# Kernel tuning notes

Hardware: AMD Instinct MI355X
Metric: run time of the kernel (lower is better)

Reference implementation:

```python
import jax, jax.numpy as jnp
import numpy as np

# Reconstructed from DAT's DAttentionBaseline with the wrapper's config:
# q_size=(14,14), n_heads=12, n_head_channels=64, n_groups=8, stride=1,
# offset_range_factor=1.0, use_pe=False (so log_cpb/rpe unused), no_off=False,
# ksize=3, dropout=0 (eval). Followed by the wrapper's Linear out-projection.

H = W = 14
G = 8          # n_groups
NH = 12        # n_heads
OFF_RANGE_FACTOR = 1.0


def grid_sample_bilinear(img, grid):
    # img: [B, C, H, W]; grid: [B, Hg, Wg, 2] in (x, y) order, [-1, 1],
    # align_corners=True, padding_mode='zeros' (torch defaults used by DAT).
    B, C, Hi, Wi = img.shape
    gx = (grid[..., 0] + 1.0) * 0.5 * (Wi - 1)
    gy = (grid[..., 1] + 1.0) * 0.5 * (Hi - 1)
    x0 = jnp.floor(gx)
    y0 = jnp.floor(gy)
    x1 = x0 + 1.0
    y1 = y0 + 1.0
    wx1 = gx - x0
    wx0 = 1.0 - wx1
    wy1 = gy - y0
    wy0 = 1.0 - wy1
    flat = img.reshape(B, C, Hi * Wi)

    def tap(xi, yi, wgt):
        valid = (xi >= 0) & (xi <= Wi - 1) & (yi >= 0) & (yi <= Hi - 1)
        xi_c = jnp.clip(xi, 0, Wi - 1).astype(jnp.int32)
        yi_c = jnp.clip(yi, 0, Hi - 1).astype(jnp.int32)
        idx = (yi_c * Wi + xi_c).reshape(B, 1, -1)
        vals = jnp.take_along_axis(flat, idx, axis=2)  # [B, C, Hg*Wg]
        w = (wgt * valid.astype(img.dtype)).reshape(B, 1, -1)
        return vals * w

    out = (tap(x0, y0, wx0 * wy0) + tap(x1, y0, wx1 * wy0)
           + tap(x0, y1, wx0 * wy1) + tap(x1, y1, wx1 * wy1))
    return out  # [B, C, Hg*Wg]


def setup_inputs() -> dict:
    key = jax.random.key(0)
    ks = jax.random.split(key, 16)
    B, N, C = 128, 196, 768
    Cg = C // G  # 96
    s = 0.02
    return {
        "hidden_states": jax.random.normal(ks[0], (B, N, C), jnp.float32),
        "Wq": jax.random.normal(ks[1], (C, C), jnp.float32) * s,
        "bq": jnp.zeros((C,), jnp.float32),
        "off_dw_w": jax.random.normal(ks[2], (Cg, 1, 3, 3), jnp.float32) * s,
        "off_dw_b": jnp.zeros((Cg,), jnp.float32),
        "ln_w": jnp.ones((Cg,), jnp.float32),
        "ln_b": jnp.zeros((Cg,), jnp.float32),
        "off_pw_w": jax.random.normal(ks[3], (2, Cg), jnp.float32) * s,
        "Wk": jax.random.normal(ks[4], (C, C), jnp.float32) * s,
        "bk": jnp.zeros((C,), jnp.float32),
        "Wv": jax.random.normal(ks[5], (C, C), jnp.float32) * s,
        "bv": jnp.zeros((C,), jnp.float32),
        "Wproj": jax.random.normal(ks[6], (C, C), jnp.float32) * s,
        "bproj": jnp.zeros((C,), jnp.float32),
        "Wout": jax.random.normal(ks[7], (C, C), jnp.float32) * s,
        "bout": jnp.zeros((C,), jnp.float32),
    }


def reference(hidden_states, Wq, bq, off_dw_w, off_dw_b, ln_w, ln_b, off_pw_w,
              Wk, bk, Wv, bv, Wproj, bproj, Wout, bout):
    B, N, C = hidden_states.shape
    Cg = C // G
    nh, dh = NH, C // NH
    scale = dh ** -0.5
    dt = hidden_states.dtype

    x_im = hidden_states.reshape(B, H, W, C).transpose(0, 3, 1, 2)  # [B,C,H,W]

    # proj_q: 1x1 conv
    q_im = jnp.einsum('bchw,oc->bohw', x_im, Wq) + bq[None, :, None, None]
    q_off = q_im.reshape(B * G, Cg, H, W)

    # offset net: depthwise 3x3 conv -> LayerNorm(channels) -> GELU -> 1x1 (no bias)
    t = jax.lax.conv_general_dilated(
        q_off, off_dw_w, (1, 1), [(1, 1), (1, 1)],
        dimension_numbers=('NCHW', 'OIHW', 'NCHW'), feature_group_count=Cg)
    t = t + off_dw_b[None, :, None, None]
    mu = t.mean(axis=1, keepdims=True)
    var = ((t - mu) ** 2).mean(axis=1, keepdims=True)
    t = (t - mu) * jax.lax.rsqrt(var + 1e-5)
    t = t * ln_w[None, :, None, None] + ln_b[None, :, None, None]
    t = jax.nn.gelu(t, approximate=False)
    off = jnp.einsum('bchw,oc->bohw', t, off_pw_w)  # [B*G, 2(y,x), H, W]

    off_range = jnp.array([1.0 / (H - 1), 1.0 / (W - 1)], dt).reshape(1, 2, 1, 1)
    off = jnp.tanh(off) * off_range * OFF_RANGE_FACTOR
    off = off.transpose(0, 2, 3, 1)  # [B*G, H, W, 2] (y, x)

    ry = ((jnp.arange(H, dtype=dt) + 0.5) / H) * 2.0 - 1.0
    rx = ((jnp.arange(W, dtype=dt) + 0.5) / W) * 2.0 - 1.0
    ref = jnp.stack(jnp.meshgrid(ry, rx, indexing='ij'), axis=-1)  # [H,W,2]
    pos = off + ref[None]          # (y, x)
    grid = pos[..., ::-1]          # (x, y) for grid_sample

    x_g = x_im.reshape(B * G, Cg, H, W)
    n_sample = H * W
    x_s = grid_sample_bilinear(x_g, grid).reshape(B, C, n_sample)

    k = jnp.einsum('bcn,oc->bon', x_s, Wk) + bk[None, :, None]
    v = jnp.einsum('bcn,oc->bon', x_s, Wv) + bv[None, :, None]

    qh = q_im.reshape(B, nh, dh, N)
    kh = k.reshape(B, nh, dh, n_sample)
    vh = v.reshape(B, nh, dh, n_sample)

    attn = jax.nn.softmax(jnp.einsum('bhcm,bhcn->bhmn', qh, kh) * scale, axis=-1)
    out = jnp.einsum('bhmn,bhcn->bhcm', attn, vh).reshape(B, C, N)

    y = jnp.einsum('bcn,oc->bon', out, Wproj) + bproj[None, :, None]
    y = y.transpose(0, 2, 1)               # [B, N, C]
    y = y @ Wout.T + bout                  # wrapper's Linear out-projection
    return y, attn
```

## Files before the change

kernel.cpp:

```cpp
#include <hip/hip_runtime.h>
#include <math.h>

#define Bsz 128
#define Hh 14
#define Ww 14
#define Nn 196
#define Cc 768
#define Gg 8
#define CgC 96
#define NHh 12
#define Dh 64
#define ROWS (Bsz*Nn)

typedef _Float16 half8 __attribute__((ext_vector_type(8)));
typedef _Float16 half4 __attribute__((ext_vector_type(4)));
typedef float f32x4 __attribute__((ext_vector_type(4)));

__global__ __launch_bounds__(256) void cvt_w5(
    const float* __restrict__ w0, const float* __restrict__ w1,
    const float* __restrict__ w2, const float* __restrict__ w3,
    const float* __restrict__ w4, _Float16* __restrict__ dst)
{
  const int i = blockIdx.x * 256 + threadIdx.x;
  const int per = Cc * Cc / 8;
  if (i >= 5 * per) return;
  const int m = i / per, r = i - m * per;
  const float* s = (m == 0) ? w0 : (m == 1) ? w1 : (m == 2) ? w2 : (m == 3) ? w3 : w4;
  float4 a = *(const float4*)(s + (size_t)r * 8);
  float4 b = *(const float4*)(s + (size_t)r * 8 + 4);
  half8 h;
  h[0]=(_Float16)a.x; h[1]=(_Float16)a.y; h[2]=(_Float16)a.z; h[3]=(_Float16)a.w;
  h[4]=(_Float16)b.x; h[5]=(_Float16)b.y; h[6]=(_Float16)b.z; h[7]=(_Float16)b.w;
  *(half8*)(dst + (size_t)m * Cc * Cc + (size_t)r * 8) = h;
}

__global__ __launch_bounds__(256) void fuse_bias(
    const float* __restrict__ Wo, const float* __restrict__ bp,
    const float* __restrict__ bo, float* __restrict__ bf)
{
  __shared__ float red[256];
  const int o2 = blockIdx.x;
  const int tid = threadIdx.x;
  const float* wrow = Wo + (size_t)o2 * Cc;
  float s = 0.f;
  for (int o = tid; o < Cc; o += 256) s = fmaf(wrow[o], bp[o], s);
  red[tid] = s;
  __syncthreads();
  for (int st = 128; st > 0; st >>= 1) { if (tid < st) red[tid] += red[tid + st]; __syncthreads(); }
  if (tid == 0) bf[o2] = red[0] + bo[o2];
}

__global__ __launch_bounds__(256) void gemm_ww(
    const _Float16* __restrict__ Wo16, const _Float16* __restrict__ Wp16,
    _Float16* __restrict__ Wf)
{
  __shared__ __align__(16) _Float16 As[128 * 64];
  __shared__ __align__(16) _Float16 Bs[128 * 72];
  const int t = threadIdx.x;
  const int bid = blockIdx.x;
  const int colb = bid % 6, rowb = bid / 6;
  const int row0 = rowb * 128, col0 = colb * 128;
  const int lane = t & 63, w = t >> 6;
  const int wr = w >> 1, wc = w & 1;
  const int l15 = lane & 15, l4 = lane >> 4;
  const int srow = t >> 3;
  const int sg   = t & 7;

  f32x4 acc[4][4];
#pragma unroll
  for (int i = 0; i < 4; ++i)
#pragma unroll
    for (int j = 0; j < 4; ++j) acc[i][j] = (f32x4){0.f, 0.f, 0.f, 0.f};

  for (int kt = 0; kt < 12; ++kt) {
    const int k0 = kt * 64;
#pragma unroll
    for (int it = 0; it < 4; ++it) {
      const int r = it * 32 + srow;
      half8 ha = *(const half8*)(Wo16 + (size_t)(row0 + r) * Cc + k0 + sg * 8);
      *(half8*)&As[r * 64 + ((sg ^ (r & 7)) * 8)] = ha;
    }
    {
      const int og = t >> 4;
      const int cg = t & 15;
#pragma unroll
      for (int it = 0; it < 4; ++it) {
        const int o = it * 16 + og;
        half8 hv = *(const half8*)(Wp16 + (size_t)(k0 + o) * Cc + col0 + cg * 8);
#pragma unroll
        for (int e = 0; e < 8; ++e)
          Bs[(cg * 8 + e) * 72 + o] = hv[e];
      }
    }
    __syncthreads();
#pragma unroll
    for (int ks = 0; ks < 2; ++ks) {
      half8 af[4], bf[4];
#pragma unroll
      for (int mi = 0; mi < 4; ++mi) {
        const int r = wr * 64 + mi * 16 + l15;
        const int g = ks * 4 + l4;
        af[mi] = *(const half8*)&As[r * 64 + ((g ^ (r & 7)) * 8)];
      }
#pragma unroll
      for (int ni = 0; ni < 4; ++ni) {
        const int c = wc * 64 + ni * 16 + l15;
        bf[ni] = *(const half8*)&Bs[c * 72 + ks * 32 + l4 * 8];
      }
#pragma unroll
      for (int mi = 0; mi < 4; ++mi)
#pragma unroll
        for (int ni = 0; ni < 4; ++ni)
          acc[mi][ni] = __builtin_amdgcn_mfma_f32_16x16x32_f16(af[mi], bf[ni], acc[mi][ni], 0, 0, 0);
    }
    __syncthreads();
  }

#pragma unroll
  for (int ni = 0; ni < 4; ++ni) {
    const int col = col0 + wc * 64 + ni * 16 + l15;
#pragma unroll
    for (int mi = 0; mi < 4; ++mi) {
      f32x4 v = acc[mi][ni];
      const int rbase = row0 + wr * 64 + mi * 16 + l4 * 4;
#pragma unroll
      for (int r = 0; r < 4; ++r)
        Wf[(size_t)(rbase + r) * Cc + col] = (_Float16)v[r];
    }
  }
}

__global__ __launch_bounds__(256) void gemm_f32a(
    const float* __restrict__ A, const _Float16* __restrict__ W,
    const float* __restrict__ bias, _Float16* __restrict__ Cout)
{
  __shared__ __align__(16) _Float16 As[128 * 64];
  __shared__ __align__(16) _Float16 Bs[128 * 64];
  const int t = threadIdx.x;
  const int nwg = gridDim.x;
  int bid = blockIdx.x;
  bid = (bid & 7) * (nwg >> 3) + (bid >> 3);
  const int colb = bid % 6, rowb = bid / 6;
  const int row0 = rowb * 128, col0 = colb * 128;
  const int lane = t & 63, w = t >> 6;
  const int wr = w >> 1, wc = w & 1;
  const int l15 = lane & 15, l4 = lane >> 4;
  const int srow = t >> 3;
  const int sg   = t & 7;

  f32x4 acc[4][4];
#pragma unroll
  for (int i = 0; i < 4; ++i)
#pragma unroll
    for (int j = 0; j < 4; ++j) acc[i][j] = (f32x4){0.f, 0.f, 0.f, 0.f};

  for (int kt = 0; kt < 12; ++kt) {
    const int k0 = kt * 64;
#pragma unroll
    for (int it = 0; it < 4; ++it) {
      const int r = it * 32 + srow;
      const float* ap = A + (size_t)(row0 + r) * Cc + k0 + sg * 8;
      float4 a0 = *(const float4*)ap;
      float4 a1 = *(const float4*)(ap + 4);
      half8 ha;
      ha[0]=(_Float16)a0.x; ha[1]=(_Float16)a0.y; ha[2]=(_Float16)a0.z; ha[3]=(_Float16)a0.w;
      ha[4]=(_Float16)a1.x; ha[5]=(_Float16)a1.y; ha[6]=(_Float16)a1.z; ha[7]=(_Float16)a1.w;
      half8 hw = *(const half8*)(W + (size_t)(col0 + r) * Cc + k0 + sg * 8);
      const int dst = r * 64 + ((sg ^ (r & 7)) * 8);
      *(half8*)&As[dst] = ha;
      *(half8*)&Bs[dst] = hw;
    }
    __syncthreads();
#pragma unroll
    for (int ks = 0; ks < 2; ++ks) {
      half8 af[4], bf[4];
#pragma unroll
      for (int mi = 0; mi < 4; ++mi) {
        const int r = wr * 64 + mi * 16 + l15;
        const int g = ks * 4 + l4;
        af[mi] = *(const half8*)&As[r * 64 + ((g ^ (r & 7)) * 8)];
      }
#pragma unroll
      for (int ni = 0; ni < 4; ++ni) {
        const int r = wc * 64 + ni * 16 + l15;
        const int g = ks * 4 + l4;
        bf[ni] = *(const half8*)&Bs[r * 64 + ((g ^ (r & 7)) * 8)];
      }
#pragma unroll
      for (int mi = 0; mi < 4; ++mi)
#pragma unroll
        for (int ni = 0; ni < 4; ++ni)
          acc[mi][ni] = __builtin_amdgcn_mfma_f32_16x16x32_f16(af[mi], bf[ni], acc[mi][ni], 0, 0, 0);
    }
    __syncthreads();
  }

#pragma unroll
  for (int ni = 0; ni < 4; ++ni) {
    const int col = col0 + wc * 64 + ni * 16 + l15;
    const float bcol = bias[col];
#pragma unroll
    for (int mi = 0; mi < 4; ++mi) {
      f32x4 v = acc[mi][ni];
      const int rbase = row0 + wr * 64 + mi * 16 + l4 * 4;
#pragma unroll
      for (int r = 0; r < 4; ++r)
        Cout[(size_t)(rbase + r) * Cc + col] = (_Float16)(v[r] + bcol);
    }
  }
}

template<int F16OUT>
__global__ __launch_bounds__(256) void gemm_h16(
    const _Float16* __restrict__ A, const _Float16* __restrict__ W,
    const float* __restrict__ bias, void* __restrict__ Cout)
{
  __shared__ __align__(16) _Float16 As[128 * 64];
  __shared__ __align__(16) _Float16 Bs[128 * 64];
  const int t = threadIdx.x;
  const int nwg = gridDim.x;
  int bid = blockIdx.x;
  bid = (bid & 7) * (nwg >> 3) + (bid >> 3);
  const int colb = bid % 6, rowb = bid / 6;
  const int row0 = rowb * 128, col0 = colb * 128;
  const int lane = t & 63, w = t >> 6;
  const int wr = w >> 1, wc = w & 1;
  const int l15 = lane & 15, l4 = lane >> 4;
  const int srow = t >> 3;
  const int sg   = t & 7;

  f32x4 acc[4][4];
#pragma unroll
  for (int i = 0; i < 4; ++i)
#pragma unroll
    for (int j = 0; j < 4; ++j) acc[i][j] = (f32x4){0.f, 0.f, 0.f, 0.f};

  for (int kt = 0; kt < 12; ++kt) {
    const int k0 = kt * 64;
#pragma unroll
    for (int it = 0; it < 4; ++it) {
      const int r = it * 32 + srow;
      half8 ha = *(const half8*)(A + (size_t)(row0 + r) * Cc + k0 + sg * 8);
      half8 hw = *(const half8*)(W + (size_t)(col0 + r) * Cc + k0 + sg * 8);
      const int dst = r * 64 + ((sg ^ (r & 7)) * 8);
      *(half8*)&As[dst] = ha;
      *(half8*)&Bs[dst] = hw;
    }
    __syncthreads();
#pragma unroll
    for (int ks = 0; ks < 2; ++ks) {
      half8 af[4], bf[4];
#pragma unroll
      for (int mi = 0; mi < 4; ++mi) {
        const int r = wr * 64 + mi * 16 + l15;
        const int g = ks * 4 + l4;
        af[mi] = *(const half8*)&As[r * 64 + ((g ^ (r & 7)) * 8)];
      }
#pragma unroll
      for (int ni = 0; ni < 4; ++ni) {
        const int r = wc * 64 + ni * 16 + l15;
        const int g = ks * 4 + l4;
        bf[ni] = *(const half8*)&Bs[r * 64 + ((g ^ (r & 7)) * 8)];
      }
#pragma unroll
      for (int mi = 0; mi < 4; ++mi)
#pragma unroll
        for (int ni = 0; ni < 4; ++ni)
          acc[mi][ni] = __builtin_amdgcn_mfma_f32_16x16x32_f16(af[mi], bf[ni], acc[mi][ni], 0, 0, 0);
    }
    __syncthreads();
  }

#pragma unroll
  for (int ni = 0; ni < 4; ++ni) {
    const int col = col0 + wc * 64 + ni * 16 + l15;
    const float bcol = bias[col];
#pragma unroll
    for (int mi = 0; mi < 4; ++mi) {
      f32x4 v = acc[mi][ni];
      const int rbase = row0 + wr * 64 + mi * 16 + l4 * 4;
#pragma unroll
      for (int r = 0; r < 4; ++r) {
        if (F16OUT) {
          ((_Float16*)Cout)[(size_t)(rbase + r) * Cc + col] = (_Float16)(v[r] + bcol);
        } else {
          ((float*)Cout)[(size_t)(rbase + r) * Cc + col] = v[r] + bcol;
        }
      }
    }
  }
}

__global__ __launch_bounds__(256) void gemm_h16_kv(
    const _Float16* __restrict__ A, const _Float16* __restrict__ Wkv,
    const float* __restrict__ bk, const float* __restrict__ bv,
    _Float16* __restrict__ K16, _Float16* __restrict__ V16)
{
  __shared__ __align__(16) _Float16 As[128 * 64];
  __shared__ __align__(16) _Float16 Bs[128 * 64];
  const int t = threadIdx.x;
  const int nwg = gridDim.x;
  int bid = blockIdx.x;
  bid = (bid & 7) * (nwg >> 3) + (bid >> 3);
  const int colb = bid % 12, rowb = bid / 12;
  const int row0 = rowb * 128, col0 = colb * 128;
  const int lane = t & 63, w = t >> 6;
  const int wr = w >> 1, wc = w & 1;
  const int l15 = lane & 15, l4 = lane >> 4;
  const int srow = t >> 3;
  const int sg   = t & 7;

  _Float16* Cout = (colb < 6) ? K16 : V16;
  const float* bias = (colb < 6) ? bk : bv;
  const int cadj = (colb < 6) ? 0 : Cc;

  f32x4 acc[4][4];
#pragma unroll
  for (int i = 0; i < 4; ++i)
#pragma unroll
    for (int j = 0; j < 4; ++j) acc[i][j] = (f32x4){0.f, 0.f, 0.f, 0.f};

  for (int kt = 0; kt < 12; ++kt) {
    const int k0 = kt * 64;
#pragma unroll
    for (int it = 0; it < 4; ++it) {
      const int r = it * 32 + srow;
      half8 ha = *(const half8*)(A + (size_t)(row0 + r) * Cc + k0 + sg * 8);
      half8 hw = *(const half8*)(Wkv + (size_t)(col0 + r) * Cc + k0 + sg * 8);
      const int dst = r * 64 + ((sg ^ (r & 7)) * 8);
      *(half8*)&As[dst] = ha;
      *(half8*)&Bs[dst] = hw;
    }
    __syncthreads();
#pragma unroll
    for (int ks = 0; ks < 2; ++ks) {
      half8 af[4], bf[4];
#pragma unroll
      for (int mi = 0; mi < 4; ++mi) {
        const int r = wr * 64 + mi * 16 + l15;
        const int g = ks * 4 + l4;
        af[mi] = *(const half8*)&As[r * 64 + ((g ^ (r & 7)) * 8)];
      }
#pragma unroll
      for (int ni = 0; ni < 4; ++ni) {
        const int r = wc * 64 + ni * 16 + l15;
        const int g = ks * 4 + l4;
        bf[ni] = *(const half8*)&Bs[r * 64 + ((g ^ (r & 7)) * 8)];
      }
#pragma unroll
      for (int mi = 0; mi < 4; ++mi)
#pragma unroll
        for (int ni = 0; ni < 4; ++ni)
          acc[mi][ni] = __builtin_amdgcn_mfma_f32_16x16x32_f16(af[mi], bf[ni], acc[mi][ni], 0, 0, 0);
    }
    __syncthreads();
  }

#pragma unroll
  for (int ni = 0; ni < 4; ++ni) {
    const int col = col0 + wc * 64 + ni * 16 + l15;
    const float bcol = bias[col - cadj];
#pragma unroll
    for (int mi = 0; mi < 4; ++mi) {
      f32x4 v = acc[mi][ni];
      const int rbase = row0 + wr * 64 + mi * 16 + l4 * 4;
#pragma unroll
      for (int r = 0; r < 4; ++r)
        Cout[(size_t)(rbase + r) * Cc + (col - cadj)] = (_Float16)(v[r] + bcol);
    }
  }
}

__global__ __launch_bounds__(512, 4) void offset_sample(
    const _Float16* __restrict__ Q16, const float* __restrict__ hidden,
    const float* __restrict__ dw_w, const float* __restrict__ dw_b,
    const float* __restrict__ ln_w, const float* __restrict__ ln_b,
    const float* __restrict__ pw_w, _Float16* __restrict__ XS)
{
  __shared__ float Qs[Nn * CgC];
  const int tid = threadIdx.x;
  const int g = blockIdx.x;
  const int b = blockIdx.y;
  const int cl = tid & 31;
  const int grp = tid >> 5;

  const size_t base = (size_t)b * Nn * Cc + g * CgC;
  for (int i = tid; i < Nn * 12; i += 512) {
    const int n = i / 12, j = i - n * 12;
    half8 hv = *(const half8*)(Q16 + base + (size_t)n * Cc + j * 8);
#pragma unroll
    for (int e = 0; e < 8; ++e) Qs[n * CgC + j * 8 + e] = (float)hv[e];
  }

  float wdw[3][9], bdw[3], wln[3], bln[3], wp0[3], wp1[3];
#pragma unroll
  for (int k = 0; k < 3; ++k) {
    const int c = cl + k * 32;
#pragma unroll
    for (int t9 = 0; t9 < 9; ++t9) wdw[k][t9] = dw_w[c * 9 + t9];
    bdw[k] = dw_b[c];
    wln[k] = ln_w[c];
    bln[k] = ln_b[c];
    wp0[k] = pw_w[c];
    wp1[k] = pw_w[CgC + c];
  }
  __syncthreads();

  const float* hb0 = hidden + base;

  for (int s0 = 0; s0 < Nn; s0 += 16) {
    const int site = s0 + grp;
    if (site >= Nn) break;
    const int h = site / Ww, w = site % Ww;

    float t[3];
#pragma unroll
    for (int k = 0; k < 3; ++k) t[k] = bdw[k];
#pragma unroll
    for (int ky = 0; ky < 3; ++ky) {
      const int hp = h + ky - 1;
      if (hp < 0 || hp > Hh - 1) continue;
#pragma unroll
      for (int kx = 0; kx < 3; ++kx) {
        const int wp = w + kx - 1;
        if (wp < 0 || wp > Ww - 1) continue;
        const float* row = &Qs[(hp * Ww + wp) * CgC + cl];
#pragma unroll
        for (int k = 0; k < 3; ++k)
          t[k] = fmaf(row[k * 32], wdw[k][ky * 3 + kx], t[k]);
      }
    }

    float s = t[0] + t[1] + t[2];
#pragma unroll
    for (int off = 1; off <= 16; off <<= 1) s += __shfl_xor(s, off, 32);
    const float mu = s * (1.f / 96.f);
    float d2 = 0.f;
#pragma unroll
    for (int k = 0; k < 3; ++k) { const float d = t[k] - mu; d2 = fmaf(d, d, d2); }
#pragma unroll
    for (int off = 1; off <= 16; off <<= 1) d2 += __shfl_xor(d2, off, 32);
    const float rstd = rsqrtf(d2 * (1.f / 96.f) + 1e-5f);

    float p0 = 0.f, p1 = 0.f;
#pragma unroll
    for (int k = 0; k < 3; ++k) {
      const float tn = (t[k] - mu) * rstd * wln[k] + bln[k];
      const float a = 0.5f * tn * (1.f + erff(tn * 0.70710678118654752f));
      p0 = fmaf(a, wp0[k], p0);
      p1 = fmaf(a, wp1[k], p1);
    }
#pragma unroll
    for (int off = 1; off <= 16; off <<= 1) {
      p0 += __shfl_xor(p0, off, 32);
      p1 += __shfl_xor(p1, off, 32);
    }

    const float offy = tanhf(p0) * (1.f / 13.f);
    const float offx = tanhf(p1) * (1.f / 13.f);
    const float refy = (h + 0.5f) / 14.f * 2.f - 1.f;
    const float refx = (w + 0.5f) / 14.f * 2.f - 1.f;
    const float gx = ((offx + refx) + 1.f) * 0.5f * 13.f;
    const float gy = ((offy + refy) + 1.f) * 0.5f * 13.f;

    const float x0f = floorf(gx), y0f = floorf(gy);
    const int x0 = (int)x0f, y0 = (int)y0f;
    const float wx1 = gx - x0f, wx0 = 1.f - wx1;
    const float wy1 = gy - y0f, wy0 = 1.f - wy1;
    const bool vx0 = (x0 >= 0) & (x0 <= 13), vx1 = (x0 + 1 >= 0) & (x0 + 1 <= 13);
    const bool vy0 = (y0 >= 0) & (y0 <= 13), vy1 = (y0 + 1 >= 0) & (y0 + 1 <= 13);
    float acc[3] = {0.f, 0.f, 0.f};
#pragma unroll
    for (int k = 0; k < 3; ++k) {
      const int c = cl + k * 32;
      if (vx0 & vy0) acc[k] = fmaf(wx0 * wy0, hb0[(size_t)(y0 * Ww + x0) * Cc + c], acc[k]);
      if (vx1 & vy0) acc[k] = fmaf(wx1 * wy0, hb0[(size_t)(y0 * Ww + x0 + 1) * Cc + c], acc[k]);
      if (vx0 & vy1) acc[k] = fmaf(wx0 * wy1, hb0[(size_t)((y0 + 1) * Ww + x0) * Cc + c], acc[k]);
      if (vx1 & vy1) acc[k] = fmaf(wx1 * wy1, hb0[(size_t)((y0 + 1) * Ww + x0 + 1) * Cc + c], acc[k]);
    }
    _Float16* xp = XS + ((size_t)b * Nn + site) * Cc + g * CgC + cl;
#pragma unroll
    for (int k = 0; k < 3; ++k) xp[k * 32] = (_Float16)acc[k];
  }
}

__global__ __launch_bounds__(512, 4) void attn_fused(
    const _Float16* __restrict__ Qm, const _Float16* __restrict__ Km,
    const _Float16* __restrict__ Vm, float* __restrict__ attn,
    _Float16* __restrict__ OUT)
{
  __shared__ __align__(16) _Float16 Kt[208 * 72];
  __shared__ __align__(16) _Float16 Vt[64 * 232];
  __shared__ __align__(16) _Float16 Ps[8][16 * 40];
  const int tid = threadIdx.x;
  const int hh = blockIdx.x, b = blockIdx.y;
  const int lane = tid & 63, wv = tid >> 6;
  const int l15 = lane & 15, l4 = lane >> 4;

  const _Float16* Qbase = Qm + (size_t)b * Nn * Cc + hh * Dh;
  const _Float16* Kbase = Km + (size_t)b * Nn * Cc + hh * Dh;
  const _Float16* Vbase = Vm + (size_t)b * Nn * Cc + hh * Dh;

  {
    const int g = tid & 7;
    for (int n = tid >> 3; n < 208; n += 64) {
      half8 hv = {};
      if (n < Nn) hv = *(const half8*)(Kbase + (size_t)n * Cc + g * 8);
      *(half8*)&Kt[n * 72 + g * 8] = hv;
    }
  }
  {
    const int d0 = (tid & 15) * 4;
    for (int n = tid >> 4; n < Nn; n += 32) {
      half4 v = *(const half4*)(Vbase + (size_t)n * Cc + d0);
      Vt[(d0 + 0) * 232 + n] = v[0];
      Vt[(d0 + 1) * 232 + n] = v[1];
      Vt[(d0 + 2) * 232 + n] = v[2];
      Vt[(d0 + 3) * 232 + n] = v[3];
    }
    for (int e = tid; e < 64 * 36; e += 512) {
      int d = e / 36, n = Nn + e % 36;
      Vt[d * 232 + n] = (_Float16)0.f;
    }
  }
  __syncthreads();

  for (int mt = wv; mt < 13; mt += 8) {
    const int qrow = mt * 16 + l15;
    const _Float16* qp = Qbase + (size_t)(qrow < Nn ? qrow : (Nn - 1)) * Cc + l4 * 8;
    half8 aq0 = *(const half8*)qp;
    half8 aq1 = *(const half8*)(qp + 32);

    f32x4 accs[13];
#pragma unroll
    for (int nt = 0; nt < 13; ++nt) accs[nt] = (f32x4){0.f, 0.f, 0.f, 0.f};
#pragma unroll
    for (int nt = 0; nt < 13; ++nt) {
      const int rb = (nt * 16 + l15) * 72;
      half8 bk0 = *(const half8*)&Kt[rb + l4 * 8];
      half8 bk1 = *(const half8*)&Kt[rb + 32 + l4 * 8];
      accs[nt] = __builtin_amdgcn_mfma_f32_16x16x32_f16(aq0, bk0, accs[nt], 0, 0, 0);
      accs[nt] = __builtin_amdgcn_mfma_f32_16x16x32_f16(aq1, bk1, accs[nt], 0, 0, 0);
    }

    float rmax[4] = {-1e30f, -1e30f, -1e30f, -1e30f};
#pragma unroll
    for (int nt = 0; nt < 13; ++nt) {
#pragma unroll
      for (int r = 0; r < 4; ++r) {
        float s = accs[nt][r] * 0.125f;
        if (nt == 12 && l15 >= 4) s = -1e30f;
        accs[nt][r] = s;
        rmax[r] = fmaxf(rmax[r], s);
      }
    }
#pragma unroll
    for (int off = 1; off <= 8; off <<= 1)
#pragma unroll
      for (int r = 0; r < 4; ++r)
        rmax[r] = fmaxf(rmax[r], __shfl_xor(rmax[r], off, 64));

    float rsum[4] = {0.f, 0.f, 0.f, 0.f};
#pragma unroll
    for (int nt = 0; nt < 13; ++nt) {
#pragma unroll
      for (int r = 0; r < 4; ++r) {
        float p = __expf(accs[nt][r] - rmax[r]);
        accs[nt][r] = p;
        rsum[r] += p;
      }
    }
#pragma unroll
    for (int off = 1; off <= 8; off <<= 1)
#pragma unroll
      for (int r = 0; r < 4; ++r)
        rsum[r] += __shfl_xor(rsum[r], off, 64);
    float rinv[4];
#pragma unroll
    for (int r = 0; r < 4; ++r) rinv[r] = 1.f / rsum[r];

    float* ab = attn + (((size_t)b * NHh + hh) * Nn) * (size_t)Nn;
#pragma unroll
    for (int nt = 0; nt < 13; ++nt) {
      const int n = nt * 16 + l15;
#pragma unroll
      for (int r = 0; r < 4; ++r) {
        float pr = accs[nt][r] * rinv[r];
        accs[nt][r] = pr;
        const int m = mt * 16 + l4 * 4 + r;
        if (m < Nn && n < Nn) ab[(size_t)m * Nn + n] = pr;
      }
    }

    f32x4 acco[4];
#pragma unroll
    for (int dt = 0; dt < 4; ++dt) acco[dt] = (f32x4){0.f, 0.f, 0.f, 0.f};
#pragma unroll
    for (int nsl = 0; nsl < 7; ++nsl) {
#pragma unroll
      for (int h2 = 0; h2 < 2; ++h2) {
        const int nt = nsl * 2 + h2;
        if (nt < 13) {
#pragma unroll
          for (int r = 0; r < 4; ++r)
            Ps[wv][(l4 * 4 + r) * 40 + h2 * 16 + l15] = (_Float16)accs[nt][r];
        } else {
#pragma unroll
          for (int r = 0; r < 4; ++r)
            Ps[wv][(l4 * 4 + r) * 40 + h2 * 16 + l15] = (_Float16)0.f;
        }
      }
      half8 ap = *(const half8*)&Ps[wv][l15 * 40 + l4 * 8];
#pragma unroll
      for (int dt = 0; dt < 4; ++dt) {
        half8 bv = *(const half8*)&Vt[(dt * 16 + l15) * 232 + nsl * 32 + l4 * 8];
        acco[dt] = __builtin_amdgcn_mfma_f32_16x16x32_f16(ap, bv, acco[dt], 0, 0, 0);
      }
    }
#pragma unroll
    for (int dt = 0; dt < 4; ++dt) {
#pragma unroll
      for (int r = 0; r < 4; ++r) {
        const int m = mt * 16 + l4 * 4 + r;
        if (m < Nn)
          OUT[((size_t)b * Nn + m) * Cc + hh * Dh + dt * 16 + l15] = (_Float16)acco[dt][r];
      }
    }
  }
}

extern "C" void kernel_launch(void* const* d_in, const int* in_sizes, int n_in,
                              void* d_out, int out_size, void* d_ws, size_t ws_size,
                              hipStream_t stream) {
  const float* hidden = (const float*)d_in[0];
  const float* Wq = (const float*)d_in[1];
  const float* bq = (const float*)d_in[2];
  const float* dw_w = (const float*)d_in[3];
  const float* dw_b = (const float*)d_in[4];
  const float* ln_w = (const float*)d_in[5];
  const float* ln_b = (const float*)d_in[6];
  const float* pw_w = (const float*)d_in[7];
  const float* Wk = (const float*)d_in[8];
  const float* bk = (const float*)d_in[9];
  const float* Wv = (const float*)d_in[10];
  const float* bv = (const float*)d_in[11];
  const float* Wp = (const float*)d_in[12];
  const float* bp = (const float*)d_in[13];
  const float* Wo = (const float*)d_in[14];
  const float* bo = (const float*)d_in[15];

  const size_t SZ = (size_t)Bsz * Nn * Cc;
  float* yout = (float*)d_out;
  float* attn = yout + SZ;

  _Float16* Q16   = (_Float16*)d_ws;
  _Float16* XS16  = Q16   + SZ;
  _Float16* K16   = XS16  + SZ;
  _Float16* V16   = K16   + SZ;
  _Float16* OUT16 = V16   + SZ;
  _Float16* W16   = OUT16 + SZ;
  _Float16* Wf16  = W16   + 5 * (size_t)Cc * Cc;
  float*    bf    = (float*)(Wf16 + (size_t)Cc * Cc);

  const int gemm_blocks = (ROWS / 128) * (Cc / 128);
  const int kv_blocks   = (ROWS / 128) * 12;

  cvt_w5<<<(5 * Cc * Cc / 8 + 255) / 256, 256, 0, stream>>>(Wq, Wk, Wv, Wp, Wo, W16);
  gemm_ww<<<36, 256, 0, stream>>>(W16 + 4 * (size_t)Cc * Cc, W16 + 3 * (size_t)Cc * Cc, Wf16);
  fuse_bias<<<Cc, 256, 0, stream>>>(Wo, bp, bo, bf);

  gemm_f32a<<<gemm_blocks, 256, 0, stream>>>(hidden, W16 + 0 * (size_t)Cc * Cc, bq, Q16);
  offset_sample<<<dim3(Gg, Bsz), 512, 0, stream>>>(Q16, hidden, dw_w, dw_b, ln_w, ln_b, pw_w, XS16);
  gemm_h16_kv<<<kv_blocks, 256, 0, stream>>>(XS16, W16 + 1 * (size_t)Cc * Cc, bk, bv, K16, V16);
  attn_fused<<<dim3(NHh, Bsz), 512, 0, stream>>>(Q16, K16, V16, attn, OUT16);
  gemm_h16<0><<<gemm_blocks, 256, 0, stream>>>(OUT16, Wf16, bf, yout);
}
```

Measured before the change: 525.4 us.

## Load GEMM tiles directly into LDS and split offset_sample across two halves

The GEMM kernels now stage their fp16 tiles with global_load_lds DMA, which writes global memory straight into shared memory and skips the register round trip. The XOR swizzle moves to the source address, so each lane fetches the chunk that belongs at its fixed LDS slot. The offset_sample kernel is split so each block handles half of the 14 spatial rows, using an 8-row Q halo. That halves its shared memory and doubles the grid, giving more occupancy and parallelism at the cost of loading the overlapping halo rows twice. The DMA path relies on the compiler inserting the correct waits before the barrier, and on gfx950 supporting 16-byte LDS loads.

Result: faster. 495.6 us, median of 3 (-5.7%).

```diff
diff --git a/kernel.cpp b/kernel.cpp
--- a/kernel.cpp
+++ b/kernel.cpp
@@ -15,6 +15,9 @@
 typedef _Float16 half8 __attribute__((ext_vector_type(8)));
 typedef _Float16 half4 __attribute__((ext_vector_type(4)));
 typedef float f32x4 __attribute__((ext_vector_type(4)));
+
+typedef __attribute__((address_space(3))) void LDSv;
+typedef __attribute__((address_space(1))) void GLBv;
 
 __global__ __launch_bounds__(256) void cvt_w5(
     const float* __restrict__ w0, const float* __restrict__ w1,
@@ -147,6 +150,8 @@
   const int l15 = lane & 15, l4 = lane >> 4;
   const int srow = t >> 3;
   const int sg   = t & 7;
+  const int rl = lane >> 3;
+  const int sl = lane & 7;
 
   f32x4 acc[4][4];
 #pragma unroll
@@ -158,6 +163,12 @@
     const int k0 = kt * 64;
 #pragma unroll
     for (int it = 0; it < 4; ++it) {
+      const int rbase = it * 32 + w * 8;
+      const int rw = rbase + rl;
+      const int sa = sl ^ (rw & 7);
+      __builtin_amdgcn_global_load_lds(
+          (GLBv*)(W + (size_t)(col0 + rw) * Cc + k0 + sa * 8),
+          (LDSv*)&Bs[rbase * 64], 16, 0, 0);
       const int r = it * 32 + srow;
       const float* ap = A + (size_t)(row0 + r) * Cc + k0 + sg * 8;
       float4 a0 = *(const float4*)ap;
@@ -165,10 +176,7 @@
       half8 ha;
       ha[0]=(_Float16)a0.x; ha[1]=(_Float16)a0.y; ha[2]=(_Float16)a0.z; ha[3]=(_Float16)a0.w;
       ha[4]=(_Float16)a1.x; ha[5]=(_Float16)a1.y; ha[6]=(_Float16)a1.z; ha[7]=(_Float16)a1.w;
-      half8 hw = *(const half8*)(W + (size_t)(col0 + r) * Cc + k0 + sg * 8);
-      const int dst = r * 64 + ((sg ^ (r & 7)) * 8);
-      *(half8*)&As[dst] = ha;
-      *(half8*)&Bs[dst] = hw;
+      *(half8*)&As[r * 64 + ((sg ^ (r & 7)) * 8)] = ha;
     }
     __syncthreads();
 #pragma unroll
@@ -226,8 +234,8 @@
   const int lane = t & 63, w = t >> 6;
   const int wr = w >> 1, wc = w & 1;
   const int l15 = lane & 15, l4 = lane >> 4;
-  const int srow = t >> 3;
-  const int sg   = t & 7;
+  const int rl = lane >> 3;
+  const int sl = lane & 7;
 
   f32x4 acc[4][4];
 #pragma unroll
@@ -239,12 +247,15 @@
     const int k0 = kt * 64;
 #pragma unroll
     for (int it = 0; it < 4; ++it) {
-      const int r = it * 32 + srow;
-      half8 ha = *(const half8*)(A + (size_t)(row0 + r) * Cc + k0 + sg * 8);
-      half8 hw = *(const half8*)(W + (size_t)(col0 + r) * Cc + k0 + sg * 8);
-      const int dst = r * 64 + ((sg ^ (r & 7)) * 8);
-      *(half8*)&As[dst] = ha;
-      *(half8*)&Bs[dst] = hw;
+      const int rbase = it * 32 + w * 8;
+      const int r = rbase + rl;
+      const int sa = sl ^ (r & 7);
+      __builtin_amdgcn_global_load_lds(
+          (GLBv*)(A + (size_t)(row0 + r) * Cc + k0 + sa * 8),
+          (LDSv*)&As[rbase * 64], 16, 0, 0);
+      __builtin_amdgcn_global_load_lds(
+          (GLBv*)(W + (size_t)(col0 + r) * Cc + k0 + sa * 8),
+          (LDSv*)&Bs[rbase * 64], 16, 0, 0);
     }
     __syncthreads();
 #pragma unroll
@@ -307,8 +318,8 @@
   const int lane = t & 63, w = t >> 6;
   const int wr = w >> 1, wc = w & 1;
   const int l15 = lane & 15, l4 = lane >> 4;
-  const int srow = t >> 3;
-  const int sg   = t & 7;
+  const int rl = lane >> 3;
+  const int sl = lane & 7;
 
   _Float16* Cout = (colb < 6) ? K16 : V16;
   const float* bias = (colb < 6) ? bk : bv;
@@ -324,12 +335,15 @@
     const int k0 = kt * 64;
 #pragma unroll
     for (int it = 0; it < 4; ++it) {
-      const int r = it * 32 + srow;
-      half8 ha = *(const half8*)(A + (size_t)(row0 + r) * Cc + k0 + sg * 8);
-      half8 hw = *(const half8*)(Wkv + (size_t)(col0 + r) * Cc + k0 + sg * 8);
-      const int dst = r * 64 + ((sg ^ (r & 7)) * 8);
-      *(half8*)&As[dst] = ha;
-      *(half8*)&Bs[dst] = hw;
+      const int rbase = it * 32 + w * 8;
+      const int r = rbase + rl;
+      const int sa = sl ^ (r & 7);
+      __builtin_amdgcn_global_load_lds(
+          (GLBv*)(A + (size_t)(row0 + r) * Cc + k0 + sa * 8),
+          (LDSv*)&As[rbase * 64], 16, 0, 0);
+      __builtin_amdgcn_global_load_lds(
+          (GLBv*)(Wkv + (size_t)(col0 + r) * Cc + k0 + sa * 8),
+          (LDSv*)&Bs[rbase * 64], 16, 0, 0);
     }
     __syncthreads();
 #pragma unroll
@@ -377,17 +391,20 @@
     const float* __restrict__ ln_w, const float* __restrict__ ln_b,
     const float* __restrict__ pw_w, _Float16* __restrict__ XS)
 {
-  __shared__ float Qs[Nn * CgC];
+  __shared__ float Qs[8 * Ww * CgC];
   const int tid = threadIdx.x;
-  const int g = blockIdx.x;
+  const int g    = blockIdx.x & 7;
+  const int half = blockIdx.x >> 3;
   const int b = blockIdx.y;
   const int cl = tid & 31;
   const int grp = tid >> 5;
+  const int hbase = half ? 6 : 0;
 
   const size_t base = (size_t)b * Nn * Cc + g * CgC;
-  for (int i = tid; i < Nn * 12; i += 512) {
+  for (int i = tid; i < 8 * Ww * 12; i += 512) {
     const int n = i / 12, j = i - n * 12;
-    half8 hv = *(const half8*)(Q16 + base + (size_t)n * Cc + j * 8);
+    const int gn = hbase * Ww + n;
+    half8 hv = *(const half8*)(Q16 + base + (size_t)gn * Cc + j * 8);
 #pragma unroll
     for (int e = 0; e < 8; ++e) Qs[n * CgC + j * 8 + e] = (float)hv[e];
   }
@@ -407,80 +424,83 @@
   __syncthreads();
 
   const float* hb0 = hidden + base;
-
-  for (int s0 = 0; s0 < Nn; s0 += 16) {
-    const int site = s0 + grp;
-    if (site >= Nn) break;
-    const int h = site / Ww, w = site % Ww;
-
-    float t[3];
-#pragma unroll
-    for (int k = 0; k < 3; ++k) t[k] = bdw[k];
-#pragma unroll
-    for (int ky = 0; ky < 3; ++ky) {
-      const int hp = h + ky - 1;
-      if (hp < 0 || hp > Hh - 1) continue;
-#pragma unroll
-      for (int kx = 0; kx < 3; ++kx) {
-        const int wp = w + kx - 1;
-        if (wp < 0 || wp > Ww - 1) continue;
-        const float* row = &Qs[(hp * Ww + wp) * CgC + cl];
-#pragma unroll
-        for (int k = 0; k < 3; ++k)
-          t[k] = fmaf(row[k * 32], wdw[k][ky * 3 + kx], t[k]);
-      }
-    }
-
-    float s = t[0] + t[1] + t[2];
-#pragma unroll
-    for (int off = 1; off <= 16; off <<= 1) s += __shfl_xor(s, off, 32);
-    const float mu = s * (1.f / 96.f);
-    float d2 = 0.f;
-#pragma unroll
-    for (int k = 0; k < 3; ++k) { const float d = t[k] - mu; d2 = fmaf(d, d, d2); }
-#pragma unroll
-    for (int off = 1; off <= 16; off <<= 1) d2 += __shfl_xor(d2, off, 32);
-    const float rstd = rsqrtf(d2 * (1.f / 96.f) + 1e-5f);
-
-    float p0 = 0.f, p1 = 0.f;
-#pragma unroll
-    for (int k = 0; k < 3; ++k) {
-      const float tn = (t[k] - mu) * rstd * wln[k] + bln[k];
-      const float a = 0.5f * tn * (1.f + erff(tn * 0.70710678118654752f));
-      p0 = fmaf(a, wp0[k], p0);
-      p1 = fmaf(a, wp1[k], p1);
-    }
-#pragma unroll
-    for (int off = 1; off <= 16; off <<= 1) {
-      p0 += __shfl_xor(p0, off, 32);
-      p1 += __shfl_xor(p1, off, 32);
-    }
-
-    const float offy = tanhf(p0) * (1.f / 13.f);
-    const float offx = tanhf(p1) * (1.f / 13.f);
-    const float refy = (h + 0.5f) / 14.f * 2.f - 1.f;
-    const float refx = (w + 0.5f) / 14.f * 2.f - 1.f;
-    const float gx = ((offx + refx) + 1.f) * 0.5f * 13.f;
-    const float gy = ((offy + refy) + 1.f) * 0.5f * 13.f;
-
-    const float x0f = floorf(gx), y0f = floorf(gy);
-    const int x0 = (int)x0f, y0 = (int)y0f;
-    const float wx1 = gx - x0f, wx0 = 1.f - wx1;
-    const float wy1 = gy - y0f, wy0 = 1.f - wy1;
-    const bool vx0 = (x0 >= 0) & (x0 <= 13), vx1 = (x0 + 1 >= 0) & (x0 + 1 <= 13);
-    const bool vy0 = (y0 >= 0) & (y0 <= 13), vy1 = (y0 + 1 >= 0) & (y0 + 1 <= 13);
-    float acc[3] = {0.f, 0.f, 0.f};
-#pragma unroll
-    for (int k = 0; k < 3; ++k) {
-      const int c = cl + k * 32;
-      if (vx0 & vy0) acc[k] = fmaf(wx0 * wy0, hb0[(size_t)(y0 * Ww + x0) * Cc + c], acc[k]);
-      if (vx1 & vy0) acc[k] = fmaf(wx1 * wy0, hb0[(size_t)(y0 * Ww + x0 + 1) * Cc + c], acc[k]);
-      if (vx0 & vy1) acc[k] = fmaf(wx0 * wy1, hb0[(size_t)((y0 + 1) * Ww + x0) * Cc + c], acc[k]);
-      if (vx1 & vy1) acc[k] = fmaf(wx1 * wy1, hb0[(size_t)((y0 + 1) * Ww + x0 + 1) * Cc + c], acc[k]);
-    }
-    _Float16* xp = XS + ((size_t)b * Nn + site) * Cc + g * CgC + cl;
-#pragma unroll
-    for (int k = 0; k < 3; ++k) xp[k * 32] = (_Float16)acc[k];
+  const int nsites = 7 * Ww;
+
+  for (int s0 = 0; s0 < nsites; s0 += 16) {
+    const int slcl = s0 + grp;
+    if (slcl < nsites) {
+      const int site = half * nsites + slcl;
+      const int h = site / Ww, w = site % Ww;
+
+      float t[3];
+#pragma unroll
+      for (int k = 0; k < 3; ++k) t[k] = bdw[k];
+#pragma unroll
+      for (int ky = 0; ky < 3; ++ky) {
+        const int hp = h + ky - 1;
+        if (hp < 0 || hp > Hh - 1) continue;
+#pragma unroll
+        for (int kx = 0; kx < 3; ++kx) {
+          const int wp = w + kx - 1;
+          if (wp < 0 || wp > Ww - 1) continue;
+          const float* row = &Qs[((hp - hbase) * Ww + wp) * CgC + cl];
+#pragma unroll
+          for (int k = 0; k < 3; ++k)
+            t[k] = fmaf(row[k * 32], wdw[k][ky * 3 + kx], t[k]);
+        }
+      }
+
+      float s = t[0] + t[1] + t[2];
+#pragma unroll
+      for (int off = 1; off <= 16; off <<= 1) s += __shfl_xor(s, off, 32);
+      const float mu = s * (1.f / 96.f);
+      float d2 = 0.f;
+#pragma unroll
+      for (int k = 0; k < 3; ++k) { const float d = t[k] - mu; d2 = fmaf(d, d, d2); }
+#pragma unroll
+      for (int off = 1; off <= 16; off <<= 1) d2 += __shfl_xor(d2, off, 32);
+      const float rstd = rsqrtf(d2 * (1.f / 96.f) + 1e-5f);
+
+      float p0 = 0.f, p1 = 0.f;
+#pragma unroll
+      for (int k = 0; k < 3; ++k) {
+        const float tn = (t[k] - mu) * rstd * wln[k] + bln[k];
+        const float a = 0.5f * tn * (1.f + erff(tn * 0.70710678118654752f));
+        p0 = fmaf(a, wp0[k], p0);
+        p1 = fmaf(a, wp1[k], p1);
+      }
+#pragma unroll
+      for (int off = 1; off <= 16; off <<= 1) {
+        p0 += __shfl_xor(p0, off, 32);
+        p1 += __shfl_xor(p1, off, 32);
+      }
+
+      const float offy = tanhf(p0) * (1.f / 13.f);
+      const float offx = tanhf(p1) * (1.f / 13.f);
+      const float refy = (h + 0.5f) / 14.f * 2.f - 1.f;
+      const float refx = (w + 0.5f) / 14.f * 2.f - 1.f;
+      const float gx = ((offx + refx) + 1.f) * 0.5f * 13.f;
+      const float gy = ((offy + refy) + 1.f) * 0.5f * 13.f;
+
+      const float x0f = floorf(gx), y0f = floorf(gy);
+      const int x0 = (int)x0f, y0 = (int)y0f;
+      const float wx1 = gx - x0f, wx0 = 1.f - wx1;
+      const float wy1 = gy - y0f, wy0 = 1.f - wy1;
+      const bool vx0 = (x0 >= 0) & (x0 <= 13), vx1 = (x0 + 1 >= 0) & (x0 + 1 <= 13);
+      const bool vy0 = (y0 >= 0) & (y0 <= 13), vy1 = (y0 + 1 >= 0) & (y0 + 1 <= 13);
+      float acc[3] = {0.f, 0.f, 0.f};
+#pragma unroll
+      for (int k = 0; k < 3; ++k) {
+        const int c = cl + k * 32;
+        if (vx0 & vy0) acc[k] = fmaf(wx0 * wy0, hb0[(size_t)(y0 * Ww + x0) * Cc + c], acc[k]);
+        if (vx1 & vy0) acc[k] = fmaf(wx1 * wy0, hb0[(size_t)(y0 * Ww + x0 + 1) * Cc + c], acc[k]);
+        if (vx0 & vy1) acc[k] = fmaf(wx0 * wy1, hb0[(size_t)((y0 + 1) * Ww + x0) * Cc + c], acc[k]);
+        if (vx1 & vy1) acc[k] = fmaf(wx1 * wy1, hb0[(size_t)((y0 + 1) * Ww + x0 + 1) * Cc + c], acc[k]);
+      }
+      _Float16* xp = XS + ((size_t)b * Nn + site) * Cc + g * CgC + cl;
+#pragma unroll
+      for (int k = 0; k < 3; ++k) xp[k * 32] = (_Float16)acc[k];
+    }
   }
 }
 
@@ -670,7 +690,7 @@
   fuse_bias<<<Cc, 256, 0, stream>>>(Wo, bp, bo, bf);
 
   gemm_f32a<<<gemm_blocks, 256, 0, stream>>>(hidden, W16 + 0 * (size_t)Cc * Cc, bq, Q16);
-  offset_sample<<<dim3(Gg, Bsz), 512, 0, stream>>>(Q16, hidden, dw_w, dw_b, ln_w, ln_b, pw_w, XS16);
+  offset_sample<<<dim3(Gg * 2, Bsz), 512, 0, stream>>>(Q16, hidden, dw_w, dw_b, ln_w, ln_b, pw_w, XS16);
   gemm_h16_kv<<<kv_blocks, 256, 0, stream>>>(XS16, W16 + 1 * (size_t)Cc * Cc, bk, bv, K16, V16);
   attn_fused<<<dim3(NHh, Bsz), 512, 0, stream>>>(Q16, K16, V16, attn, OUT16);
   gemm_h16<0><<<gemm_blocks, 256, 0, stream>>>(OUT16, Wf16, bf, yout);
```
